# Kernel optimization log

Hardware: AMD Instinct MI355X
Metric: run time of the kernel (lower is better)

The kernel has to match this reference:

```python
import jax, jax.numpy as jnp
import numpy as np

N = 100000
E = 1600000
IN = 128
H = 256
K = 7          # n_hops + 1
INTERVAL = 3
R = K - INTERVAL + 1  # n_relations + 1 = 5


def setup_inputs() -> dict:
    key = jax.random.key(0)
    ks = jax.random.split(key, 8)
    features = jax.random.normal(ks[0], (N, IN), dtype=jnp.float32)
    W1 = jax.random.normal(ks[1], (K, IN, H), dtype=jnp.float32) * (1.0 / np.sqrt(IN))
    b1 = jnp.zeros((K, H), dtype=jnp.float32)
    W2 = jax.random.normal(ks[2], (K, H, H), dtype=jnp.float32) * (1.0 / np.sqrt(H))
    b2 = jnp.zeros((K, H), dtype=jnp.float32)
    Wr = jax.random.normal(ks[3], (R, H * INTERVAL, H), dtype=jnp.float32) * (1.0 / np.sqrt(H * INTERVAL))
    br = jnp.zeros((R, H), dtype=jnp.float32)
    row = jax.random.randint(ks[4], (E,), 0, N, dtype=jnp.int64)
    col = jax.random.randint(ks[5], (E,), 0, N, dtype=jnp.int64)
    return {"features": features, "W1": W1, "b1": b1, "W2": W2, "b2": b2,
            "Wr": Wr, "br": br, "row": row, "col": col}


def _norm_adj(row, col):
    # set_diag=True: add self loops; symm_norm: D^-1/2 (A+I) D^-1/2
    diag = jnp.arange(N, dtype=row.dtype)
    r = jnp.concatenate([row, diag])
    c = jnp.concatenate([col, diag])
    deg = jax.ops.segment_sum(jnp.ones_like(r, dtype=jnp.float32), r, num_segments=N)
    dinv = jnp.where(deg > 0, jax.lax.rsqrt(deg), 0.0)
    w = dinv[r] * dinv[c]  # [E+N]
    return r, c, w


def _forward(features, W1, b1, W2, b2, Wr, br, row, col):
    r, c, w = _norm_adj(row, col)

    def spmm(x):  # x: [N, F] -> A_hat @ x
        return jax.ops.segment_sum(x[c] * w[:, None], r, num_segments=N)

    def step(x, _):
        nx = spmm(x)
        return nx, nx

    _, hops = jax.lax.scan(step, features, None, length=K - 1)  # [K-1, N, IN]
    hop_feats = jnp.concatenate([features[None], hops], axis=0)  # [K, N, IN]

    # per-hop DeepSets (2-layer MLP with ReLU): [K, N, H]
    h = jax.nn.relu(jnp.einsum('kni,kih->knh', hop_feats, W1) + b1[:, None, :])
    h = jnp.einsum('knh,khg->kng', h, W2) + b2[:, None, :]

    hops_feats = jnp.transpose(h, (1, 0, 2))  # [N, K, H]
    # sliding windows of INTERVAL hops: [R, N, INTERVAL*H]
    wins = jnp.stack([hops_feats[:, i:i + INTERVAL, :].reshape(N, INTERVAL * H)
                      for i in range(R)], axis=0)
    rel = jax.nn.relu(jnp.einsum('rnd,rdh->rnh', wins, Wr) + br[:, None, :])  # [R, N, H]
    out = jnp.transpose(rel, (1, 0, 2)).reshape(N, R * H)  # concat over relations
    return out


def reference(features, W1, b1, W2, b2, Wr, br, row, col):
    return _forward(features, W1, b1, W2, b2, Wr, br, row, col)
```

## Files before the change

kernel.cpp:

```cpp
#include <hip/hip_runtime.h>

#define N_NODES 100000
#define E_EDGES 1600000
#define IN_F 128
#define H_F 256
#define K_HOPS 7
#define R_REL 5
#define OUT_W (R_REL * H_F)

typedef __attribute__((ext_vector_type(8))) short short8;
typedef __attribute__((ext_vector_type(4))) float f32x4;


__global__ void zero_int(int* __restrict__ p, int n) {
    int t = blockIdx.x * blockDim.x + threadIdx.x;
    if (t < n) p[t] = 0;
}

__global__ void deg_count(const int* __restrict__ row, int* __restrict__ deg) {
    int e = blockIdx.x * blockDim.x + threadIdx.x;
    if (e < E_EDGES) atomicAdd(&deg[row[e]], 1);
}

__global__ void dinv_compute(const int* __restrict__ deg, float* __restrict__ dinv) {
    int i = blockIdx.x * blockDim.x + threadIdx.x;
    if (i < N_NODES) dinv[i] = rsqrtf((float)(deg[i] + 1));
}

__global__ __launch_bounds__(1024) void exscan_rowptr(const int* __restrict__ deg,
                                                      int* __restrict__ rowptr) {
    __shared__ int wsum[16];
    __shared__ int carry_s;
    const int t = threadIdx.x, lane = t & 63, wv = t >> 6;
    if (t == 0) carry_s = 0;
    __syncthreads();
    for (int base = 0; base < N_NODES; base += 1024) {
        int i = base + t;
        int v = (i < N_NODES) ? deg[i] : 0;
        int x = v;
#pragma unroll
        for (int off = 1; off < 64; off <<= 1) {
            int n = __shfl_up(x, off, 64);
            if (lane >= off) x += n;
        }
        if (lane == 63) wsum[wv] = x;
        __syncthreads();
        if (wv == 0 && lane < 16) {
            int s = wsum[lane];
#pragma unroll
            for (int off = 1; off < 16; off <<= 1) {
                int n = __shfl_up(s, off, 64);
                if (lane >= off) s += n;
            }
            wsum[lane] = s;
        }
        __syncthreads();
        int wbase = (wv == 0) ? 0 : wsum[wv - 1];
        if (i < N_NODES) rowptr[i] = carry_s + wbase + x - v;
        __syncthreads();
        if (t == 1023) carry_s += wsum[15];
        __syncthreads();
    }
    if (threadIdx.x == 0) rowptr[N_NODES] = carry_s;
}

__global__ void csr_scatter(const int* __restrict__ row, const int* __restrict__ col,
                            const float* __restrict__ dinv, const int* __restrict__ rowptr,
                            int* __restrict__ cursor, int* __restrict__ cols2,
                            float* __restrict__ ew) {
    int e = blockIdx.x * blockDim.x + threadIdx.x;
    if (e >= E_EDGES) return;
    int r = row[e], c = col[e];
    int pos = rowptr[r] + atomicAdd(&cursor[r], 1);
    cols2[pos] = c;
    ew[pos] = dinv[r] * dinv[c];
}

__global__ __launch_bounds__(256) void spmm_csr(
    const float2* __restrict__ x, const int* __restrict__ rowptr,
    const int* __restrict__ cols, const float* __restrict__ w,
    const float* __restrict__ dinv, float2* __restrict__ y) {
    const int wave = threadIdx.x >> 6, lane = threadIdx.x & 63;
    const int i = blockIdx.x * 4 + wave;
    if (i >= N_NODES) return;
    const float d = dinv[i];
    float2 xv = x[(size_t)i * 64 + lane];
    float2 acc;
    acc.x = d * d * xv.x;
    acc.y = d * d * xv.y;
    int j = rowptr[i];
    const int e = rowptr[i + 1];
    for (; j + 3 < e; j += 4) {
        int c0 = cols[j], c1 = cols[j + 1], c2 = cols[j + 2], c3 = cols[j + 3];
        float w0 = w[j], w1 = w[j + 1], w2 = w[j + 2], w3 = w[j + 3];
        float2 v0 = x[(size_t)c0 * 64 + lane];
        float2 v1 = x[(size_t)c1 * 64 + lane];
        float2 v2 = x[(size_t)c2 * 64 + lane];
        float2 v3 = x[(size_t)c3 * 64 + lane];
        acc.x += w0 * v0.x + w1 * v1.x + w2 * v2.x + w3 * v3.x;
        acc.y += w0 * v0.y + w1 * v1.y + w2 * v2.y + w3 * v3.y;
    }
    for (; j < e; ++j) {
        int c0 = cols[j];
        float w0 = w[j];
        float2 v0 = x[(size_t)c0 * 64 + lane];
        acc.x += w0 * v0.x;
        acc.y += w0 * v0.y;
    }
    y[(size_t)i * 64 + lane] = acc;
}

__global__ __launch_bounds__(256) void wc_compute(const float* __restrict__ W2,
                                                  const float* __restrict__ Wr,
                                                  float* __restrict__ Wc) {
    const int z = blockIdx.x, j = blockIdx.y, g = threadIdx.x;
    const int r = z / 3, d = z % 3, hop = r + d;
    const float* a = W2 + (size_t)hop * H_F * H_F + (size_t)j * H_F;
    const float* b = Wr + ((size_t)r * 768 + (size_t)d * H_F) * H_F + g;
    float acc = 0.f;
#pragma unroll 4
    for (int h = 0; h < H_F; ++h) acc += a[h] * b[(size_t)h * H_F];
    Wc[(size_t)z * H_F * H_F + (size_t)j * H_F + g] = acc;
}

__global__ __launch_bounds__(256) void bc_compute(const float* __restrict__ b2,
                                                  const float* __restrict__ Wr,
                                                  const float* __restrict__ br,
                                                  float* __restrict__ bc) {
    const int r = blockIdx.x, g = threadIdx.x;
    float acc = br[(size_t)r * H_F + g];
    for (int t = 0; t < 3 * H_F; ++t) {
        float bv = b2[(size_t)(r + t / H_F) * H_F + (t % H_F)];
        acc += bv * Wr[((size_t)r * 768 + t) * H_F + g];
    }
    bc[(size_t)r * H_F + g] = acc;
}


__device__ __forceinline__ void f2bf_split(float v, short& h, short& l) {
    unsigned u = __float_as_uint(v);
    unsigned hb = (u + 0x7FFFu + ((u >> 16) & 1u)) >> 16;
    float fh = __uint_as_float(hb << 16);
    float r = v - fh;
    unsigned u2 = __float_as_uint(r);
    unsigned lb = (u2 + 0x7FFFu + ((u2 >> 16) & 1u)) >> 16;
    h = (short)(unsigned short)hb;
    l = (short)(unsigned short)lb;
}

__global__ void transpose_convert(const float* __restrict__ in, short* __restrict__ oh,
                                  short* __restrict__ ol, int Kd, int grp) {
    __shared__ float t[32][33];
    const int i0 = blockIdx.x * 32, n0 = blockIdx.y * 32, z = blockIdx.z;
    const int tx = threadIdx.x, ty = threadIdx.y;
    const int outLd = grp * Kd;
    const float* ip = in + (size_t)z * Kd * 256;
#pragma unroll
    for (int j = 0; j < 4; ++j)
        t[ty + 8 * j][tx] = ip[(size_t)(i0 + ty + 8 * j) * 256 + n0 + tx];
    __syncthreads();
    size_t base = (size_t)(z / grp) * 256 * outLd + (size_t)(z % grp) * Kd;
#pragma unroll
    for (int j = 0; j < 4; ++j) {
        float v = t[tx][ty + 8 * j];
        short hb, lb;
        f2bf_split(v, hb, lb);
        size_t o = base + (size_t)(n0 + ty + 8 * j) * outLd + i0 + tx;
        oh[o] = hb;
        ol[o] = lb;
    }
}


#define LROW 40

template <int MODE>
__global__ __launch_bounds__(256, 2) void gemm_split(
    const float* __restrict__ A, int lda, long hopStride,
    const short* __restrict__ BTh, const short* __restrict__ BTl, int ldb, int Kd,
    float* __restrict__ C, int ldc, const float* __restrict__ bias, int M)
{
    __shared__ short lds_buf[4 * 128 * LROW];
    short* Ah = lds_buf;
    short* Al = lds_buf + 128 * LROW;
    short* Bh = lds_buf + 2 * 128 * LROW;
    short* Bl = lds_buf + 3 * 128 * LROW;

    const int tid = threadIdx.x;
    const int lane = tid & 63, wave = tid >> 6;
    const int wm = wave & 1, wn = wave >> 1;
    const int fr = lane & 15, fg = lane >> 4;
    const int m0 = blockIdx.y * 128;
    const int n0 = blockIdx.x * 128;

    const int sr = tid >> 1;
    const int sc = (tid & 1) * 16;
    const bool avalid = (m0 + sr) < M;
    const int arow = avalid ? (m0 + sr) : (M - 1);

    f32x4 ga[4];
    short8 gbh[2], gbl[2];

    {
        const float* ap = A + (size_t)arow * lda + sc;
        const short* bph = BTh + (size_t)(n0 + sr) * ldb + sc;
        const short* bpl = BTl + (size_t)(n0 + sr) * ldb + sc;
#pragma unroll
        for (int l = 0; l < 4; ++l) ga[l] = *(const f32x4*)(ap + 4 * l);
        gbh[0] = *(const short8*)bph;  gbh[1] = *(const short8*)(bph + 8);
        gbl[0] = *(const short8*)bpl;  gbl[1] = *(const short8*)(bpl + 8);
    }

    f32x4 acc[4][4];
#pragma unroll
    for (int i = 0; i < 4; ++i)
#pragma unroll
        for (int j = 0; j < 4; ++j) acc[i][j] = (f32x4)0.f;

    const int nk = Kd / 32;
    for (int kk = 0; kk < nk; ++kk) {
        __syncthreads();
        {
            short8 vh[2], vl[2];
#pragma unroll
            for (int l = 0; l < 4; ++l) {
                f32x4 v = ga[l];
                if (!avalid) v = (f32x4)0.f;
#pragma unroll
                for (int e = 0; e < 4; ++e) {
                    short hb, lb;
                    f2bf_split(v[e], hb, lb);
                    vh[l >> 1][(l & 1) * 4 + e] = hb;
                    vl[l >> 1][(l & 1) * 4 + e] = lb;
                }
            }
            *(short8*)(Ah + sr * LROW + sc)     = vh[0];
            *(short8*)(Ah + sr * LROW + sc + 8) = vh[1];
            *(short8*)(Al + sr * LROW + sc)     = vl[0];
            *(short8*)(Al + sr * LROW + sc + 8) = vl[1];
            *(short8*)(Bh + sr * LROW + sc)     = gbh[0];
            *(short8*)(Bh + sr * LROW + sc + 8) = gbh[1];
            *(short8*)(Bl + sr * LROW + sc)     = gbl[0];
            *(short8*)(Bl + sr * LROW + sc + 8) = gbl[1];
        }
        __syncthreads();

        if (kk + 1 < nk) {
            int k0 = (kk + 1) * 32;
            const float* ap = A + (size_t)(k0 >> 8) * hopStride + (k0 & 255)
                              + (size_t)arow * lda + sc;
            const short* bph = BTh + (size_t)(n0 + sr) * ldb + k0 + sc;
            const short* bpl = BTl + (size_t)(n0 + sr) * ldb + k0 + sc;
#pragma unroll
            for (int l = 0; l < 4; ++l) ga[l] = *(const f32x4*)(ap + 4 * l);
            gbh[0] = *(const short8*)bph;  gbh[1] = *(const short8*)(bph + 8);
            gbl[0] = *(const short8*)bpl;  gbl[1] = *(const short8*)(bpl + 8);
        }

        short8 afh[4], afl[4], bfh[4], bfl[4];
#pragma unroll
        for (int mf = 0; mf < 4; ++mf) {
            int r = wm * 64 + mf * 16 + fr;
            afh[mf] = *(const short8*)(Ah + r * LROW + fg * 8);
            afl[mf] = *(const short8*)(Al + r * LROW + fg * 8);
        }
#pragma unroll
        for (int nf = 0; nf < 4; ++nf) {
            int r = wn * 64 + nf * 16 + fr;
            bfh[nf] = *(const short8*)(Bh + r * LROW + fg * 8);
            bfl[nf] = *(const short8*)(Bl + r * LROW + fg * 8);
        }
#pragma unroll
        for (int mf = 0; mf < 4; ++mf)
#pragma unroll
            for (int nf = 0; nf < 4; ++nf) {
                acc[mf][nf] = __builtin_amdgcn_mfma_f32_16x16x32_bf16(
                    afh[mf], bfh[nf], acc[mf][nf], 0, 0, 0);
                acc[mf][nf] = __builtin_amdgcn_mfma_f32_16x16x32_bf16(
                    afh[mf], bfl[nf], acc[mf][nf], 0, 0, 0);
                acc[mf][nf] = __builtin_amdgcn_mfma_f32_16x16x32_bf16(
                    afl[mf], bfh[nf], acc[mf][nf], 0, 0, 0);
            }
    }

#pragma unroll
    for (int nf = 0; nf < 4; ++nf) {
        int colg = n0 + wn * 64 + nf * 16 + fr;
        float bv = (MODE <= 1) ? bias[colg] : 0.f;
#pragma unroll
        for (int mf = 0; mf < 4; ++mf) {
            int rowbase = m0 + wm * 64 + mf * 16 + fg * 4;
#pragma unroll
            for (int j = 0; j < 4; ++j) {
                int rowg = rowbase + j;
                if (rowg < M) {
                    float* cp = C + (size_t)rowg * ldc + colg;
                    float v = acc[mf][nf][j] + bv;
                    if (MODE >= 2) v += *cp;
                    if (MODE & 1) v = fmaxf(v, 0.f);
                    *cp = v;
                }
            }
        }
    }
}

template <int MODE>
static void launch_gemm(const float* A, int lda, long hopStride,
                        const short* BTh, const short* BTl, int ldb, int Kd,
                        float* C, int ldc, const float* bias, int M, hipStream_t s) {
    dim3 grid(2, (M + 127) / 128);
    gemm_split<MODE><<<grid, 256, 0, s>>>(A, lda, hopStride, BTh, BTl, ldb, Kd,
                                          C, ldc, bias, M);
}


extern "C" void kernel_launch(void* const* d_in, const int* in_sizes, int n_in,
                              void* d_out, int out_size, void* d_ws, size_t ws_size,
                              hipStream_t stream) {
    const float* features = (const float*)d_in[0];
    const float* W1 = (const float*)d_in[1];
    const float* b1 = (const float*)d_in[2];
    const float* W2 = (const float*)d_in[3];
    const float* b2 = (const float*)d_in[4];
    const float* Wr = (const float*)d_in[5];
    const float* br = (const float*)d_in[6];
    const int* row = (const int*)d_in[7];
    const int* col = (const int*)d_in[8];
    float* out = (float*)d_out;

    char* ws = (char*)d_ws;
    int* deg = (int*)ws;
    int* rowptr = (int*)(ws + (1ull << 20));
    float* dinv = (float*)(ws + (2ull << 20));
    int* cols2 = (int*)(ws + (4ull << 20));
    float* ew = (float*)(ws + (11ull << 20));
    short* w1h = (short*)(ws + (18ull << 20));
    short* w1l = (short*)(ws + (19ull << 20));
    float* wc32 = (float*)(ws + (20ull << 20));
    short* wch = (short*)(ws + (24ull << 20));
    short* wcl = (short*)(ws + (26ull << 20));
    float* bc = (float*)(ws + (28ull << 20));
    float* xa = (float*)(ws + (32ull << 20));
    float* xb = (float*)(ws + (96ull << 20));
    float* h1 = (float*)(ws + (160ull << 20));

    const bool windowed = ws_size >= (1000ull << 20);

    zero_int<<<(N_NODES + 255) / 256, 256, 0, stream>>>(deg, N_NODES);
    deg_count<<<(E_EDGES + 255) / 256, 256, 0, stream>>>(row, deg);
    dinv_compute<<<(N_NODES + 255) / 256, 256, 0, stream>>>(deg, dinv);
    exscan_rowptr<<<1, 1024, 0, stream>>>(deg, rowptr);
    zero_int<<<(N_NODES + 255) / 256, 256, 0, stream>>>(deg, N_NODES);
    csr_scatter<<<(E_EDGES + 255) / 256, 256, 0, stream>>>(row, col, dinv, rowptr,
                                                           deg, cols2, ew);

    wc_compute<<<dim3(15, H_F), 256, 0, stream>>>(W2, Wr, wc32);
    bc_compute<<<R_REL, 256, 0, stream>>>(b2, Wr, br, bc);

    dim3 tb(32, 8);
    transpose_convert<<<dim3(IN_F / 32, 8, K_HOPS), tb, 0, stream>>>(W1, w1h, w1l, IN_F, 1);
    transpose_convert<<<dim3(H_F / 32, 8, 15), tb, 0, stream>>>(wc32, wch, wcl, H_F, 3);

    const float* xcur = features;
    float* bufs[2] = {xa, xb};
    for (int k = 0; k < K_HOPS; ++k) {
        float* h1dst = windowed ? (h1 + (size_t)k * N_NODES * H_F) : h1;
        launch_gemm<1>(xcur, IN_F, 0, w1h + (size_t)k * 256 * IN_F,
                       w1l + (size_t)k * 256 * IN_F, IN_F, IN_F,
                       h1dst, H_F, b1 + (size_t)k * H_F, N_NODES, stream);

        if (!windowed) {
            int rlo = (k - 2 < 0) ? 0 : (k - 2);
            int rhi = (k < R_REL - 1) ? k : (R_REL - 1);
            for (int r = rlo; r <= rhi; ++r) {
                int d = k - r;
                const short* Bh = wch + (size_t)r * 256 * 768 + (size_t)d * H_F;
                const short* Bl = wcl + (size_t)r * 256 * 768 + (size_t)d * H_F;
                float* Cp = out + (size_t)r * H_F;
                if (k == r)
                    launch_gemm<0>(h1, H_F, 0, Bh, Bl, 768, H_F, Cp, OUT_W,
                                   bc + (size_t)r * H_F, N_NODES, stream);
                else if (k == r + 2)
                    launch_gemm<3>(h1, H_F, 0, Bh, Bl, 768, H_F, Cp, OUT_W,
                                   nullptr, N_NODES, stream);
                else
                    launch_gemm<2>(h1, H_F, 0, Bh, Bl, 768, H_F, Cp, OUT_W,
                                   nullptr, N_NODES, stream);
            }
        }

        if (k < K_HOPS - 1) {
            float* xn = bufs[k & 1];
            spmm_csr<<<(N_NODES + 3) / 4, 256, 0, stream>>>(
                (const float2*)xcur, rowptr, cols2, ew, dinv, (float2*)xn);
            xcur = xn;
        }
    }

    if (windowed) {
        for (int r = 0; r < R_REL; ++r) {
            launch_gemm<1>(h1 + (size_t)r * N_NODES * H_F, H_F, (long)N_NODES * H_F,
                           wch + (size_t)r * 256 * 768, wcl + (size_t)r * 256 * 768,
                           768, 768, out + (size_t)r * H_F, OUT_W,
                           bc + (size_t)r * H_F, N_NODES, stream);
        }
    }
}
```

Baseline: 2.450 ms.

## Pre-split GEMM A operands into bf16 hi/lo in producers instead of per-tile

The GEMM now reads activations that were already split into bf16 high/low halves. The split is done by the SpMM epilogue, by a new split_pack kernel for the input features, and by the first-layer GEMM epilogue, which now writes h1 as hi/lo shorts. This removes the repeated per-tile float-to-bf16 split inside the GEMM main loop. The GEMM A-tile loads shrink from fp32 to two bf16 arrays, and h1 storage is halved per array. The cost is extra hi/lo writes from SpMM and one extra conversion pass. The h1 workspace layout is also shifted, with the windowed path taking about 700MB for h1h/h1l.

Result: slower. 2.747 ms (+12.1%).

```diff
diff --git a/kernel.cpp b/kernel.cpp
--- a/kernel.cpp
+++ b/kernel.cpp
@@ -76,10 +76,41 @@
     ew[pos] = dinv[r] * dinv[c];
 }
 
+
+__device__ __forceinline__ void f2bf_split(float v, short& h, short& l) {
+    unsigned u = __float_as_uint(v);
+    unsigned hb = (u + 0x7FFFu + ((u >> 16) & 1u)) >> 16;
+    float fh = __uint_as_float(hb << 16);
+    float r = v - fh;
+    unsigned u2 = __float_as_uint(r);
+    unsigned lb = (u2 + 0x7FFFu + ((u2 >> 16) & 1u)) >> 16;
+    h = (short)(unsigned short)hb;
+    l = (short)(unsigned short)lb;
+}
+
+__device__ __forceinline__ int pack2(short a, short b) {
+    return (int)(unsigned short)a | ((int)(unsigned short)b << 16);
+}
+
+__global__ void split_pack(const float4* __restrict__ in, int2* __restrict__ oh,
+                           int2* __restrict__ ol, int n4) {
+    int t = blockIdx.x * blockDim.x + threadIdx.x;
+    if (t >= n4) return;
+    float4 v = in[t];
+    short h0, l0, h1, l1, h2, l2, h3, l3;
+    f2bf_split(v.x, h0, l0);
+    f2bf_split(v.y, h1, l1);
+    f2bf_split(v.z, h2, l2);
+    f2bf_split(v.w, h3, l3);
+    oh[t] = make_int2(pack2(h0, h1), pack2(h2, h3));
+    ol[t] = make_int2(pack2(l0, l1), pack2(l2, l3));
+}
+
 __global__ __launch_bounds__(256) void spmm_csr(
     const float2* __restrict__ x, const int* __restrict__ rowptr,
     const int* __restrict__ cols, const float* __restrict__ w,
-    const float* __restrict__ dinv, float2* __restrict__ y) {
+    const float* __restrict__ dinv, float2* __restrict__ y,
+    int* __restrict__ yh, int* __restrict__ yl) {
     const int wave = threadIdx.x >> 6, lane = threadIdx.x & 63;
     const int i = blockIdx.x * 4 + wave;
     if (i >= N_NODES) return;
@@ -108,6 +139,11 @@
         acc.y += w0 * v0.y;
     }
     y[(size_t)i * 64 + lane] = acc;
+    short hx, lx, hy, ly;
+    f2bf_split(acc.x, hx, lx);
+    f2bf_split(acc.y, hy, ly);
+    yh[(size_t)i * 64 + lane] = pack2(hx, hy);
+    yl[(size_t)i * 64 + lane] = pack2(lx, ly);
 }
 
 __global__ __launch_bounds__(256) void wc_compute(const float* __restrict__ W2,
@@ -136,18 +172,6 @@
     bc[(size_t)r * H_F + g] = acc;
 }
 
-
-__device__ __forceinline__ void f2bf_split(float v, short& h, short& l) {
-    unsigned u = __float_as_uint(v);
-    unsigned hb = (u + 0x7FFFu + ((u >> 16) & 1u)) >> 16;
-    float fh = __uint_as_float(hb << 16);
-    float r = v - fh;
-    unsigned u2 = __float_as_uint(r);
-    unsigned lb = (u2 + 0x7FFFu + ((u2 >> 16) & 1u)) >> 16;
-    h = (short)(unsigned short)hb;
-    l = (short)(unsigned short)lb;
-}
-
 __global__ void transpose_convert(const float* __restrict__ in, short* __restrict__ oh,
                                   short* __restrict__ ol, int Kd, int grp) {
     __shared__ float t[32][33];
@@ -174,11 +198,12 @@
 
 #define LROW 40
 
-template <int MODE>
+template <int MODE, bool OUTSPLIT>
 __global__ __launch_bounds__(256, 2) void gemm_split(
-    const float* __restrict__ A, int lda, long hopStride,
+    const short* __restrict__ Agh, const short* __restrict__ Agl, int lda, long hopStride,
     const short* __restrict__ BTh, const short* __restrict__ BTl, int ldb, int Kd,
-    float* __restrict__ C, int ldc, const float* __restrict__ bias, int M)
+    float* __restrict__ C, short* __restrict__ Ch, short* __restrict__ Cl, int ldc,
+    const float* __restrict__ bias, int M)
 {
     __shared__ short lds_buf[4 * 128 * LROW];
     short* Ah = lds_buf;
@@ -198,15 +223,15 @@
     const bool avalid = (m0 + sr) < M;
     const int arow = avalid ? (m0 + sr) : (M - 1);
 
-    f32x4 ga[4];
-    short8 gbh[2], gbl[2];
+    short8 gah[2], gal[2], gbh[2], gbl[2];
 
     {
-        const float* ap = A + (size_t)arow * lda + sc;
+        const short* aph = Agh + (size_t)arow * lda + sc;
+        const short* apl = Agl + (size_t)arow * lda + sc;
         const short* bph = BTh + (size_t)(n0 + sr) * ldb + sc;
         const short* bpl = BTl + (size_t)(n0 + sr) * ldb + sc;
-#pragma unroll
-        for (int l = 0; l < 4; ++l) ga[l] = *(const f32x4*)(ap + 4 * l);
+        gah[0] = *(const short8*)aph;  gah[1] = *(const short8*)(aph + 8);
+        gal[0] = *(const short8*)apl;  gal[1] = *(const short8*)(apl + 8);
         gbh[0] = *(const short8*)bph;  gbh[1] = *(const short8*)(bph + 8);
         gbl[0] = *(const short8*)bpl;  gbl[1] = *(const short8*)(bpl + 8);
     }
@@ -220,39 +245,26 @@
     const int nk = Kd / 32;
     for (int kk = 0; kk < nk; ++kk) {
         __syncthreads();
-        {
-            short8 vh[2], vl[2];
-#pragma unroll
-            for (int l = 0; l < 4; ++l) {
-                f32x4 v = ga[l];
-                if (!avalid) v = (f32x4)0.f;
-#pragma unroll
-                for (int e = 0; e < 4; ++e) {
-                    short hb, lb;
-                    f2bf_split(v[e], hb, lb);
-                    vh[l >> 1][(l & 1) * 4 + e] = hb;
-                    vl[l >> 1][(l & 1) * 4 + e] = lb;
-                }
-            }
-            *(short8*)(Ah + sr * LROW + sc)     = vh[0];
-            *(short8*)(Ah + sr * LROW + sc + 8) = vh[1];
-            *(short8*)(Al + sr * LROW + sc)     = vl[0];
-            *(short8*)(Al + sr * LROW + sc + 8) = vl[1];
-            *(short8*)(Bh + sr * LROW + sc)     = gbh[0];
-            *(short8*)(Bh + sr * LROW + sc + 8) = gbh[1];
-            *(short8*)(Bl + sr * LROW + sc)     = gbl[0];
-            *(short8*)(Bl + sr * LROW + sc + 8) = gbl[1];
-        }
+        *(short8*)(Ah + sr * LROW + sc)     = gah[0];
+        *(short8*)(Ah + sr * LROW + sc + 8) = gah[1];
+        *(short8*)(Al + sr * LROW + sc)     = gal[0];
+        *(short8*)(Al + sr * LROW + sc + 8) = gal[1];
+        *(short8*)(Bh + sr * LROW + sc)     = gbh[0];
+        *(short8*)(Bh + sr * LROW + sc + 8) = gbh[1];
+        *(short8*)(Bl + sr * LROW + sc)     = gbl[0];
+        *(short8*)(Bl + sr * LROW + sc + 8) = gbl[1];
         __syncthreads();
 
         if (kk + 1 < nk) {
             int k0 = (kk + 1) * 32;
-            const float* ap = A + (size_t)(k0 >> 8) * hopStride + (k0 & 255)
-                              + (size_t)arow * lda + sc;
+            const short* aph = Agh + (size_t)(k0 >> 8) * hopStride + (k0 & 255)
+                               + (size_t)arow * lda + sc;
+            const short* apl = Agl + (size_t)(k0 >> 8) * hopStride + (k0 & 255)
+                               + (size_t)arow * lda + sc;
             const short* bph = BTh + (size_t)(n0 + sr) * ldb + k0 + sc;
             const short* bpl = BTl + (size_t)(n0 + sr) * ldb + k0 + sc;
-#pragma unroll
-            for (int l = 0; l < 4; ++l) ga[l] = *(const f32x4*)(ap + 4 * l);
+            gah[0] = *(const short8*)aph;  gah[1] = *(const short8*)(aph + 8);
+            gal[0] = *(const short8*)apl;  gal[1] = *(const short8*)(apl + 8);
             gbh[0] = *(const short8*)bph;  gbh[1] = *(const short8*)(bph + 8);
             gbl[0] = *(const short8*)bpl;  gbl[1] = *(const short8*)(bpl + 8);
         }
@@ -294,24 +306,32 @@
             for (int j = 0; j < 4; ++j) {
                 int rowg = rowbase + j;
                 if (rowg < M) {
-                    float* cp = C + (size_t)rowg * ldc + colg;
                     float v = acc[mf][nf][j] + bv;
-                    if (MODE >= 2) v += *cp;
+                    size_t idx = (size_t)rowg * ldc + colg;
+                    if (MODE >= 2) v += C[idx];
                     if (MODE & 1) v = fmaxf(v, 0.f);
-                    *cp = v;
+                    if (OUTSPLIT) {
+                        short hb, lb;
+                        f2bf_split(v, hb, lb);
+                        Ch[idx] = hb;
+                        Cl[idx] = lb;
+                    } else {
+                        C[idx] = v;
+                    }
                 }
             }
         }
     }
 }
 
-template <int MODE>
-static void launch_gemm(const float* A, int lda, long hopStride,
+template <int MODE, bool OSPL>
+static void launch_gemm(const short* Agh, const short* Agl, int lda, long hopStride,
                         const short* BTh, const short* BTl, int ldb, int Kd,
-                        float* C, int ldc, const float* bias, int M, hipStream_t s) {
+                        float* C, short* Ch, short* Cl, int ldc,
+                        const float* bias, int M, hipStream_t s) {
     dim3 grid(2, (M + 127) / 128);
-    gemm_split<MODE><<<grid, 256, 0, s>>>(A, lda, hopStride, BTh, BTl, ldb, Kd,
-                                          C, ldc, bias, M);
+    gemm_split<MODE, OSPL><<<grid, 256, 0, s>>>(Agh, Agl, lda, hopStride, BTh, BTl,
+                                                ldb, Kd, C, Ch, Cl, ldc, bias, M);
 }
 
 
@@ -343,7 +363,10 @@
     float* bc = (float*)(ws + (28ull << 20));
     float* xa = (float*)(ws + (32ull << 20));
     float* xb = (float*)(ws + (96ull << 20));
-    float* h1 = (float*)(ws + (160ull << 20));
+    short* xh = (short*)(ws + (160ull << 20));
+    short* xl = (short*)(ws + (192ull << 20));
+    short* h1h = (short*)(ws + (224ull << 20));
+    short* h1l = (short*)(ws + (576ull << 20));
 
     const bool windowed = ws_size >= (1000ull << 20);
 
@@ -362,13 +385,21 @@
     transpose_convert<<<dim3(IN_F / 32, 8, K_HOPS), tb, 0, stream>>>(W1, w1h, w1l, IN_F, 1);
     transpose_convert<<<dim3(H_F / 32, 8, 15), tb, 0, stream>>>(wc32, wch, wcl, H_F, 3);
 
+    {
+        int n4 = N_NODES * IN_F / 4;
+        split_pack<<<(n4 + 255) / 256, 256, 0, stream>>>(
+            (const float4*)features, (int2*)xh, (int2*)xl, n4);
+    }
+
     const float* xcur = features;
     float* bufs[2] = {xa, xb};
     for (int k = 0; k < K_HOPS; ++k) {
-        float* h1dst = windowed ? (h1 + (size_t)k * N_NODES * H_F) : h1;
-        launch_gemm<1>(xcur, IN_F, 0, w1h + (size_t)k * 256 * IN_F,
-                       w1l + (size_t)k * 256 * IN_F, IN_F, IN_F,
-                       h1dst, H_F, b1 + (size_t)k * H_F, N_NODES, stream);
+        short* h1hd = windowed ? (h1h + (size_t)k * N_NODES * H_F) : h1h;
+        short* h1ld = windowed ? (h1l + (size_t)k * N_NODES * H_F) : h1l;
+        launch_gemm<1, true>(xh, xl, IN_F, 0,
+                             w1h + (size_t)k * 256 * IN_F, w1l + (size_t)k * 256 * IN_F,
+                             IN_F, IN_F, nullptr, h1hd, h1ld, H_F,
+                             b1 + (size_t)k * H_F, N_NODES, stream);
 
         if (!windowed) {
             int rlo = (k - 2 < 0) ? 0 : (k - 2);
@@ -379,31 +410,37 @@
                 const short* Bl = wcl + (size_t)r * 256 * 768 + (size_t)d * H_F;
                 float* Cp = out + (size_t)r * H_F;
                 if (k == r)
-                    launch_gemm<0>(h1, H_F, 0, Bh, Bl, 768, H_F, Cp, OUT_W,
-                                   bc + (size_t)r * H_F, N_NODES, stream);
+                    launch_gemm<0, false>(h1h, h1l, H_F, 0, Bh, Bl, 768, H_F,
+                                          Cp, nullptr, nullptr, OUT_W,
+                                          bc + (size_t)r * H_F, N_NODES, stream);
                 else if (k == r + 2)
-                    launch_gemm<3>(h1, H_F, 0, Bh, Bl, 768, H_F, Cp, OUT_W,
-                                   nullptr, N_NODES, stream);
+                    launch_gemm<3, false>(h1h, h1l, H_F, 0, Bh, Bl, 768, H_F,
+                                          Cp, nullptr, nullptr, OUT_W,
+                                          nullptr, N_NODES, stream);
                 else
-                    launch_gemm<2>(h1, H_F, 0, Bh, Bl, 768, H_F, Cp, OUT_W,
-                                   nullptr, N_NODES, stream);
+                    launch_gemm<2, false>(h1h, h1l, H_F, 0, Bh, Bl, 768, H_F,
+                                          Cp, nullptr, nullptr, OUT_W,
+                                          nullptr, N_NODES, stream);
             }
         }
 
         if (k < K_HOPS - 1) {
             float* xn = bufs[k & 1];
             spmm_csr<<<(N_NODES + 3) / 4, 256, 0, stream>>>(
-                (const float2*)xcur, rowptr, cols2, ew, dinv, (float2*)xn);
+                (const float2*)xcur, rowptr, cols2, ew, dinv, (float2*)xn,
+                (int*)xh, (int*)xl);
             xcur = xn;
         }
     }
 
     if (windowed) {
         for (int r = 0; r < R_REL; ++r) {
-            launch_gemm<1>(h1 + (size_t)r * N_NODES * H_F, H_F, (long)N_NODES * H_F,
-                           wch + (size_t)r * 256 * 768, wcl + (size_t)r * 256 * 768,
-                           768, 768, out + (size_t)r * H_F, OUT_W,
-                           bc + (size_t)r * H_F, N_NODES, stream);
-        }
-    }
-}
+            launch_gemm<1, false>(h1h + (size_t)r * N_NODES * H_F,
+                                  h1l + (size_t)r * N_NODES * H_F, H_F,
+                                  (long)N_NODES * H_F,
+                                  wch + (size_t)r * 256 * 768, wcl + (size_t)r * 256 * 768,
+                                  768, 768, out + (size_t)r * H_F, nullptr, nullptr, OUT_W,
+                                  bc + (size_t)r * H_F, N_NODES, stream);
+        }
+    }
+}
```

## Pre-split hidden activations to bf16 hi/lo and pipeline relation GEMM via direct-to-LDS loads

Applied to the files above, without the earlier changes.

The first-layer GEMM now writes its ReLU output as pre-split bf16 hi/lo halves, so downstream relation GEMMs no longer convert fp32 to split bf16 on every tile load. The windowed relation GEMM becomes a single launch over all relations and uses double-buffered LDS filled by global_load_lds with a swizzled layout, overlapping loads with MFMA work. The hi/lo storage keeps the intermediate the same size as fp32 and needs a new workspace layout. The wider grid also changes scheduling.

After: 2.437 ms. About the same (-0.5%).

```diff
diff --git a/kernel.cpp b/kernel.cpp
--- a/kernel.cpp
+++ b/kernel.cpp
@@ -10,6 +10,10 @@
 
 typedef __attribute__((ext_vector_type(8))) short short8;
 typedef __attribute__((ext_vector_type(4))) float f32x4;
+
+#define GLOAD16(g, l) __builtin_amdgcn_global_load_lds( \
+    (const __attribute__((address_space(1))) void*)(g), \
+    (__attribute__((address_space(3))) void*)(l), 16, 0, 0)
 
 
 __global__ void zero_int(int* __restrict__ p, int n) {
@@ -110,6 +114,18 @@
     y[(size_t)i * 64 + lane] = acc;
 }
 
+
+__device__ __forceinline__ void f2bf_split(float v, short& h, short& l) {
+    unsigned u = __float_as_uint(v);
+    unsigned hb = (u + 0x7FFFu + ((u >> 16) & 1u)) >> 16;
+    float fh = __uint_as_float(hb << 16);
+    float r = v - fh;
+    unsigned u2 = __float_as_uint(r);
+    unsigned lb = (u2 + 0x7FFFu + ((u2 >> 16) & 1u)) >> 16;
+    h = (short)(unsigned short)hb;
+    l = (short)(unsigned short)lb;
+}
+
 __global__ __launch_bounds__(256) void wc_compute(const float* __restrict__ W2,
                                                   const float* __restrict__ Wr,
                                                   float* __restrict__ Wc) {
@@ -136,18 +152,6 @@
     bc[(size_t)r * H_F + g] = acc;
 }
 
-
-__device__ __forceinline__ void f2bf_split(float v, short& h, short& l) {
-    unsigned u = __float_as_uint(v);
-    unsigned hb = (u + 0x7FFFu + ((u >> 16) & 1u)) >> 16;
-    float fh = __uint_as_float(hb << 16);
-    float r = v - fh;
-    unsigned u2 = __float_as_uint(r);
-    unsigned lb = (u2 + 0x7FFFu + ((u2 >> 16) & 1u)) >> 16;
-    h = (short)(unsigned short)hb;
-    l = (short)(unsigned short)lb;
-}
-
 __global__ void transpose_convert(const float* __restrict__ in, short* __restrict__ oh,
                                   short* __restrict__ ol, int Kd, int grp) {
     __shared__ float t[32][33];
@@ -174,9 +178,257 @@
 
 #define LROW 40
 
+__global__ __launch_bounds__(256, 2) void gemm_mlp(
+    const float* __restrict__ A,
+    const short* __restrict__ BTh, const short* __restrict__ BTl,
+    short* __restrict__ Ch, short* __restrict__ Cl,
+    const float* __restrict__ bias, int M)
+{
+    __shared__ short lds_buf[4 * 128 * LROW];
+    short* Ah = lds_buf;
+    short* Al = lds_buf + 128 * LROW;
+    short* Bh = lds_buf + 2 * 128 * LROW;
+    short* Bl = lds_buf + 3 * 128 * LROW;
+
+    const int tid = threadIdx.x;
+    const int lane = tid & 63, wave = tid >> 6;
+    const int wm = wave & 1, wn = wave >> 1;
+    const int fr = lane & 15, fg = lane >> 4;
+    const int m0 = blockIdx.y * 128;
+    const int n0 = blockIdx.x * 128;
+
+    const int sr = tid >> 1;
+    const int sc = (tid & 1) * 16;
+    const bool avalid = (m0 + sr) < M;
+    const int arow = avalid ? (m0 + sr) : (M - 1);
+
+    f32x4 ga[4];
+    short8 gbh[2], gbl[2];
+    {
+        const float* ap = A + (size_t)arow * IN_F + sc;
+        const short* bph = BTh + (size_t)(n0 + sr) * IN_F + sc;
+        const short* bpl = BTl + (size_t)(n0 + sr) * IN_F + sc;
+#pragma unroll
+        for (int l = 0; l < 4; ++l) ga[l] = *(const f32x4*)(ap + 4 * l);
+        gbh[0] = *(const short8*)bph;  gbh[1] = *(const short8*)(bph + 8);
+        gbl[0] = *(const short8*)bpl;  gbl[1] = *(const short8*)(bpl + 8);
+    }
+
+    f32x4 acc[4][4];
+#pragma unroll
+    for (int i = 0; i < 4; ++i)
+#pragma unroll
+        for (int j = 0; j < 4; ++j) acc[i][j] = (f32x4)0.f;
+
+    const int nk = IN_F / 32;
+    for (int kk = 0; kk < nk; ++kk) {
+        __syncthreads();
+        {
+            short8 vh[2], vl[2];
+#pragma unroll
+            for (int l = 0; l < 4; ++l) {
+                f32x4 v = ga[l];
+                if (!avalid) v = (f32x4)0.f;
+#pragma unroll
+                for (int e = 0; e < 4; ++e) {
+                    short hb, lb;
+                    f2bf_split(v[e], hb, lb);
+                    vh[l >> 1][(l & 1) * 4 + e] = hb;
+                    vl[l >> 1][(l & 1) * 4 + e] = lb;
+                }
+            }
+            *(short8*)(Ah + sr * LROW + sc)     = vh[0];
+            *(short8*)(Ah + sr * LROW + sc + 8) = vh[1];
+            *(short8*)(Al + sr * LROW + sc)     = vl[0];
+            *(short8*)(Al + sr * LROW + sc + 8) = vl[1];
+            *(short8*)(Bh + sr * LROW + sc)     = gbh[0];
+            *(short8*)(Bh + sr * LROW + sc + 8) = gbh[1];
+            *(short8*)(Bl + sr * LROW + sc)     = gbl[0];
+            *(short8*)(Bl + sr * LROW + sc + 8) = gbl[1];
+        }
+        __syncthreads();
+
+        if (kk + 1 < nk) {
+            int k0 = (kk + 1) * 32;
+            const float* ap = A + (size_t)arow * IN_F + k0 + sc;
+            const short* bph = BTh + (size_t)(n0 + sr) * IN_F + k0 + sc;
+            const short* bpl = BTl + (size_t)(n0 + sr) * IN_F + k0 + sc;
+#pragma unroll
+            for (int l = 0; l < 4; ++l) ga[l] = *(const f32x4*)(ap + 4 * l);
+            gbh[0] = *(const short8*)bph;  gbh[1] = *(const short8*)(bph + 8);
+            gbl[0] = *(const short8*)bpl;  gbl[1] = *(const short8*)(bpl + 8);
+        }
+
+        short8 afh[4], afl[4], bfh[4], bfl[4];
+#pragma unroll
+        for (int mf = 0; mf < 4; ++mf) {
+            int r = wm * 64 + mf * 16 + fr;
+            afh[mf] = *(const short8*)(Ah + r * LROW + fg * 8);
+            afl[mf] = *(const short8*)(Al + r * LROW + fg * 8);
+        }
+#pragma unroll
+        for (int nf = 0; nf < 4; ++nf) {
+            int r = wn * 64 + nf * 16 + fr;
+            bfh[nf] = *(const short8*)(Bh + r * LROW + fg * 8);
+            bfl[nf] = *(const short8*)(Bl + r * LROW + fg * 8);
+        }
+#pragma unroll
+        for (int mf = 0; mf < 4; ++mf)
+#pragma unroll
+            for (int nf = 0; nf < 4; ++nf) {
+                acc[mf][nf] = __builtin_amdgcn_mfma_f32_16x16x32_bf16(
+                    afh[mf], bfh[nf], acc[mf][nf], 0, 0, 0);
+                acc[mf][nf] = __builtin_amdgcn_mfma_f32_16x16x32_bf16(
+                    afh[mf], bfl[nf], acc[mf][nf], 0, 0, 0);
+                acc[mf][nf] = __builtin_amdgcn_mfma_f32_16x16x32_bf16(
+                    afl[mf], bfh[nf], acc[mf][nf], 0, 0, 0);
+            }
+    }
+
+#pragma unroll
+    for (int nf = 0; nf < 4; ++nf) {
+        int colg = n0 + wn * 64 + nf * 16 + fr;
+        float bv = bias[colg];
+#pragma unroll
+        for (int mf = 0; mf < 4; ++mf) {
+            int rowbase = m0 + wm * 64 + mf * 16 + fg * 4;
+#pragma unroll
+            for (int j = 0; j < 4; ++j) {
+                int rowg = rowbase + j;
+                if (rowg < M) {
+                    float v = fmaxf(acc[mf][nf][j] + bv, 0.f);
+                    short hb, lb;
+                    f2bf_split(v, hb, lb);
+                    size_t idx = (size_t)rowg * H_F + colg;
+                    Ch[idx] = hb;
+                    Cl[idx] = lb;
+                }
+            }
+        }
+    }
+}
+
+
+__global__ __launch_bounds__(256, 2) void gemm_rel(
+    const short* __restrict__ h1h, const short* __restrict__ h1l, long hopStride,
+    const short* __restrict__ wch, const short* __restrict__ wcl,
+    float* __restrict__ outB, const float* __restrict__ bcB, int M)
+{
+    __shared__ short lds[2][4][128 * 32];
+
+    const int tid = threadIdx.x;
+    const int lane = tid & 63, wave = tid >> 6;
+    const int wm = wave & 1, wn = wave >> 1;
+    const int fr = lane & 15, fg = lane >> 4;
+    const int m0 = blockIdx.y * 128;
+    const int n0 = blockIdx.x * 128;
+    const int rrel = blockIdx.z;
+
+    const short* Agh = h1h + (size_t)rrel * hopStride;
+    const short* Agl = h1l + (size_t)rrel * hopStride;
+    const short* BTh = wch + (size_t)rrel * 256 * 768;
+    const short* BTl = wcl + (size_t)rrel * 256 * 768;
+    float* C = outB + (size_t)rrel * H_F;
+    const float* bias = bcB + (size_t)rrel * H_F;
+
+    int aoff[2], boff[2], loff[2];
+#pragma unroll
+    for (int q = 0; q < 2; ++q) {
+        int c = wave * 2 + q;
+        int r = c * 16 + (lane >> 2);
+        int u = lane & 3;
+        int g = (u - (r >> 1)) & 3;
+        int ar = m0 + r; if (ar >= M) ar = M - 1;
+        aoff[q] = ar * H_F + g * 8;
+        boff[q] = (n0 + r) * 768 + g * 8;
+        loff[q] = c * 512;
+    }
+
+#define STAGE_REL(buf, kg) do {                                                  \
+        int hop_ = (kg) >> 8, kin_ = (kg) & 255;                                 \
+        const short* ah_ = Agh + (size_t)hop_ * hopStride + kin_;                \
+        const short* al_ = Agl + (size_t)hop_ * hopStride + kin_;                \
+        const short* bh_ = BTh + (kg);                                           \
+        const short* bl_ = BTl + (kg);                                           \
+        GLOAD16(ah_ + aoff[0], &lds[buf][0][loff[0]]);                           \
+        GLOAD16(ah_ + aoff[1], &lds[buf][0][loff[1]]);                           \
+        GLOAD16(al_ + aoff[0], &lds[buf][1][loff[0]]);                           \
+        GLOAD16(al_ + aoff[1], &lds[buf][1][loff[1]]);                           \
+        GLOAD16(bh_ + boff[0], &lds[buf][2][loff[0]]);                           \
+        GLOAD16(bh_ + boff[1], &lds[buf][2][loff[1]]);                           \
+        GLOAD16(bl_ + boff[0], &lds[buf][3][loff[0]]);                           \
+        GLOAD16(bl_ + boff[1], &lds[buf][3][loff[1]]);                           \
+    } while (0)
+
+    f32x4 acc[4][4];
+#pragma unroll
+    for (int i = 0; i < 4; ++i)
+#pragma unroll
+        for (int j = 0; j < 4; ++j) acc[i][j] = (f32x4)0.f;
+
+    STAGE_REL(0, 0);
+    __syncthreads();
+
+    int cur = 0;
+    const int nk = 768 / 32;
+    for (int kt = 0; kt < nk; ++kt) {
+        if (kt + 1 < nk) STAGE_REL(cur ^ 1, (kt + 1) * 32);
+
+        const short* Ahc = &lds[cur][0][0];
+        const short* Alc = &lds[cur][1][0];
+        const short* Bhc = &lds[cur][2][0];
+        const short* Blc = &lds[cur][3][0];
+
+        short8 bfh[4], bfl[4];
+#pragma unroll
+        for (int nf = 0; nf < 4; ++nf) {
+            int rb = wn * 64 + nf * 16 + fr;
+            int ub = (fg + (rb >> 1)) & 3;
+            bfh[nf] = *(const short8*)(Bhc + rb * 32 + ub * 8);
+            bfl[nf] = *(const short8*)(Blc + rb * 32 + ub * 8);
+        }
+#pragma unroll
+        for (int mf = 0; mf < 4; ++mf) {
+            int ra = wm * 64 + mf * 16 + fr;
+            int ua = (fg + (ra >> 1)) & 3;
+            short8 ah = *(const short8*)(Ahc + ra * 32 + ua * 8);
+            short8 al = *(const short8*)(Alc + ra * 32 + ua * 8);
+#pragma unroll
+            for (int nf = 0; nf < 4; ++nf) {
+                acc[mf][nf] = __builtin_amdgcn_mfma_f32_16x16x32_bf16(
+                    ah, bfh[nf], acc[mf][nf], 0, 0, 0);
+                acc[mf][nf] = __builtin_amdgcn_mfma_f32_16x16x32_bf16(
+                    ah, bfl[nf], acc[mf][nf], 0, 0, 0);
+                acc[mf][nf] = __builtin_amdgcn_mfma_f32_16x16x32_bf16(
+                    al, bfh[nf], acc[mf][nf], 0, 0, 0);
+            }
+        }
+        __syncthreads();
+        cur ^= 1;
+    }
+
+#pragma unroll
+    for (int nf = 0; nf < 4; ++nf) {
+        int colg = n0 + wn * 64 + nf * 16 + fr;
+        float bv = bias[colg];
+#pragma unroll
+        for (int mf = 0; mf < 4; ++mf) {
+            int rowbase = m0 + wm * 64 + mf * 16 + fg * 4;
+#pragma unroll
+            for (int j = 0; j < 4; ++j) {
+                int rowg = rowbase + j;
+                if (rowg < M)
+                    C[(size_t)rowg * OUT_W + colg] = fmaxf(acc[mf][nf][j] + bv, 0.f);
+            }
+        }
+    }
+#undef STAGE_REL
+}
+
+
 template <int MODE>
-__global__ __launch_bounds__(256, 2) void gemm_split(
-    const float* __restrict__ A, int lda, long hopStride,
+__global__ __launch_bounds__(256, 2) void gemm_presplit(
+    const short* __restrict__ Agh, const short* __restrict__ Agl, int lda,
     const short* __restrict__ BTh, const short* __restrict__ BTl, int ldb, int Kd,
     float* __restrict__ C, int ldc, const float* __restrict__ bias, int M)
 {
@@ -198,15 +450,14 @@
     const bool avalid = (m0 + sr) < M;
     const int arow = avalid ? (m0 + sr) : (M - 1);
 
-    f32x4 ga[4];
-    short8 gbh[2], gbl[2];
-
+    short8 gah[2], gal[2], gbh[2], gbl[2];
     {
-        const float* ap = A + (size_t)arow * lda + sc;
+        const short* aph = Agh + (size_t)arow * lda + sc;
+        const short* apl = Agl + (size_t)arow * lda + sc;
         const short* bph = BTh + (size_t)(n0 + sr) * ldb + sc;
         const short* bpl = BTl + (size_t)(n0 + sr) * ldb + sc;
-#pragma unroll
-        for (int l = 0; l < 4; ++l) ga[l] = *(const f32x4*)(ap + 4 * l);
+        gah[0] = *(const short8*)aph;  gah[1] = *(const short8*)(aph + 8);
+        gal[0] = *(const short8*)apl;  gal[1] = *(const short8*)(apl + 8);
         gbh[0] = *(const short8*)bph;  gbh[1] = *(const short8*)(bph + 8);
         gbl[0] = *(const short8*)bpl;  gbl[1] = *(const short8*)(bpl + 8);
     }
@@ -220,39 +471,24 @@
     const int nk = Kd / 32;
     for (int kk = 0; kk < nk; ++kk) {
         __syncthreads();
-        {
-            short8 vh[2], vl[2];
-#pragma unroll
-            for (int l = 0; l < 4; ++l) {
-                f32x4 v = ga[l];
-                if (!avalid) v = (f32x4)0.f;
-#pragma unroll
-                for (int e = 0; e < 4; ++e) {
-                    short hb, lb;
-                    f2bf_split(v[e], hb, lb);
-                    vh[l >> 1][(l & 1) * 4 + e] = hb;
-                    vl[l >> 1][(l & 1) * 4 + e] = lb;
-                }
-            }
-            *(short8*)(Ah + sr * LROW + sc)     = vh[0];
-            *(short8*)(Ah + sr * LROW + sc + 8) = vh[1];
-            *(short8*)(Al + sr * LROW + sc)     = vl[0];
-            *(short8*)(Al + sr * LROW + sc + 8) = vl[1];
-            *(short8*)(Bh + sr * LROW + sc)     = gbh[0];
-            *(short8*)(Bh + sr * LROW + sc + 8) = gbh[1];
-            *(short8*)(Bl + sr * LROW + sc)     = gbl[0];
-            *(short8*)(Bl + sr * LROW + sc + 8) = gbl[1];
-        }
+        *(short8*)(Ah + sr * LROW + sc)     = gah[0];
+        *(short8*)(Ah + sr * LROW + sc + 8) = gah[1];
+        *(short8*)(Al + sr * LROW + sc)     = gal[0];
+        *(short8*)(Al + sr * LROW + sc + 8) = gal[1];
+        *(short8*)(Bh + sr * LROW + sc)     = gbh[0];
+        *(short8*)(Bh + sr * LROW + sc + 8) = gbh[1];
+        *(short8*)(Bl + sr * LROW + sc)     = gbl[0];
+        *(short8*)(Bl + sr * LROW + sc + 8) = gbl[1];
         __syncthreads();
 
         if (kk + 1 < nk) {
             int k0 = (kk + 1) * 32;
-            const float* ap = A + (size_t)(k0 >> 8) * hopStride + (k0 & 255)
-                              + (size_t)arow * lda + sc;
+            const short* aph = Agh + (size_t)arow * lda + k0 + sc;
+            const short* apl = Agl + (size_t)arow * lda + k0 + sc;
             const short* bph = BTh + (size_t)(n0 + sr) * ldb + k0 + sc;
             const short* bpl = BTl + (size_t)(n0 + sr) * ldb + k0 + sc;
-#pragma unroll
-            for (int l = 0; l < 4; ++l) ga[l] = *(const f32x4*)(ap + 4 * l);
+            gah[0] = *(const short8*)aph;  gah[1] = *(const short8*)(aph + 8);
+            gal[0] = *(const short8*)apl;  gal[1] = *(const short8*)(apl + 8);
             gbh[0] = *(const short8*)bph;  gbh[1] = *(const short8*)(bph + 8);
             gbl[0] = *(const short8*)bpl;  gbl[1] = *(const short8*)(bpl + 8);
         }
@@ -286,7 +522,7 @@
 #pragma unroll
     for (int nf = 0; nf < 4; ++nf) {
         int colg = n0 + wn * 64 + nf * 16 + fr;
-        float bv = (MODE <= 1) ? bias[colg] : 0.f;
+        float bv = (MODE == 0) ? bias[colg] : 0.f;
 #pragma unroll
         for (int mf = 0; mf < 4; ++mf) {
             int rowbase = m0 + wm * 64 + mf * 16 + fg * 4;
@@ -294,24 +530,15 @@
             for (int j = 0; j < 4; ++j) {
                 int rowg = rowbase + j;
                 if (rowg < M) {
-                    float* cp = C + (size_t)rowg * ldc + colg;
+                    size_t idx = (size_t)rowg * ldc + colg;
                     float v = acc[mf][nf][j] + bv;
-                    if (MODE >= 2) v += *cp;
+                    if (MODE >= 2) v += C[idx];
                     if (MODE & 1) v = fmaxf(v, 0.f);
-                    *cp = v;
+                    C[idx] = v;
                 }
             }
         }
     }
-}
-
-template <int MODE>
-static void launch_gemm(const float* A, int lda, long hopStride,
-                        const short* BTh, const short* BTl, int ldb, int Kd,
-                        float* C, int ldc, const float* bias, int M, hipStream_t s) {
-    dim3 grid(2, (M + 127) / 128);
-    gemm_split<MODE><<<grid, 256, 0, s>>>(A, lda, hopStride, BTh, BTl, ldb, Kd,
-                                          C, ldc, bias, M);
 }
 
 
@@ -343,7 +570,8 @@
     float* bc = (float*)(ws + (28ull << 20));
     float* xa = (float*)(ws + (32ull << 20));
     float* xb = (float*)(ws + (96ull << 20));
-    float* h1 = (float*)(ws + (160ull << 20));
+    short* h1h = (short*)(ws + (160ull << 20));
+    short* h1l = (short*)(ws + (576ull << 20));
 
     const bool windowed = ws_size >= (1000ull << 20);
 
@@ -365,10 +593,12 @@
     const float* xcur = features;
     float* bufs[2] = {xa, xb};
     for (int k = 0; k < K_HOPS; ++k) {
-        float* h1dst = windowed ? (h1 + (size_t)k * N_NODES * H_F) : h1;
-        launch_gemm<1>(xcur, IN_F, 0, w1h + (size_t)k * 256 * IN_F,
-                       w1l + (size_t)k * 256 * IN_F, IN_F, IN_F,
-                       h1dst, H_F, b1 + (size_t)k * H_F, N_NODES, stream);
+        short* h1hd = windowed ? (h1h + (size_t)k * N_NODES * H_F) : h1h;
+        short* h1ld = windowed ? (h1l + (size_t)k * N_NODES * H_F) : h1l;
+        dim3 grid(2, (N_NODES + 127) / 128);
+        gemm_mlp<<<grid, 256, 0, stream>>>(xcur, w1h + (size_t)k * 256 * IN_F,
+                                           w1l + (size_t)k * 256 * IN_F,
+                                           h1hd, h1ld, b1 + (size_t)k * H_F, N_NODES);
 
         if (!windowed) {
             int rlo = (k - 2 < 0) ? 0 : (k - 2);
@@ -379,14 +609,15 @@
                 const short* Bl = wcl + (size_t)r * 256 * 768 + (size_t)d * H_F;
                 float* Cp = out + (size_t)r * H_F;
                 if (k == r)
-                    launch_gemm<0>(h1, H_F, 0, Bh, Bl, 768, H_F, Cp, OUT_W,
-                                   bc + (size_t)r * H_F, N_NODES, stream);
+                    gemm_presplit<0><<<grid, 256, 0, stream>>>(
+                        h1h, h1l, H_F, Bh, Bl, 768, H_F, Cp, OUT_W,
+                        bc + (size_t)r * H_F, N_NODES);
                 else if (k == r + 2)
-                    launch_gemm<3>(h1, H_F, 0, Bh, Bl, 768, H_F, Cp, OUT_W,
-                                   nullptr, N_NODES, stream);
+                    gemm_presplit<3><<<grid, 256, 0, stream>>>(
+                        h1h, h1l, H_F, Bh, Bl, 768, H_F, Cp, OUT_W, nullptr, N_NODES);
                 else
-                    launch_gemm<2>(h1, H_F, 0, Bh, Bl, 768, H_F, Cp, OUT_W,
-                                   nullptr, N_NODES, stream);
+                    gemm_presplit<2><<<grid, 256, 0, stream>>>(
+                        h1h, h1l, H_F, Bh, Bl, 768, H_F, Cp, OUT_W, nullptr, N_NODES);
             }
         }
 
@@ -399,11 +630,8 @@
     }
 
     if (windowed) {
-        for (int r = 0; r < R_REL; ++r) {
-            launch_gemm<1>(h1 + (size_t)r * N_NODES * H_F, H_F, (long)N_NODES * H_F,
-                           wch + (size_t)r * 256 * 768, wcl + (size_t)r * 256 * 768,
-                           768, 768, out + (size_t)r * H_F, OUT_W,
-                           bc + (size_t)r * H_F, N_NODES, stream);
-        }
-    }
-}
+        dim3 grid(2, (N_NODES + 127) / 128, R_REL);
+        gemm_rel<<<grid, 256, 0, stream>>>(h1h, h1l, (long)N_NODES * H_F,
+                                           wch, wcl, out, bc, N_NODES);
+    }
+}
```
